# Kernel tuning notes

Measured on AMD Instinct MI355X. Metric: run time of the kernel, lower is better.

The kernel has to match this reference:

```python
import jax, jax.numpy as jnp
import numpy as np

DIM = 128
N_GNN = 3
B, N1, N2 = 8, 128, 512
VDW_N = 6.0
DEV_VDW = 0.2
MAX_VDW, MIN_VDW = 0.0356, 0.0178
DM_MIN = 0.5


def setup_inputs() -> dict:
    key = jax.random.key(0)
    ks = jax.random.split(key, 24)
    f32 = jnp.float32
    h1 = jax.random.normal(ks[0], (B, N1, 54), f32)
    h2 = jax.random.normal(ks[1], (B, N2, 54), f32)
    a1 = (jax.random.uniform(ks[2], (B, N1, N1)) < 0.1).astype(f32)
    adj1 = jnp.clip(a1 + jnp.swapaxes(a1, 1, 2) + jnp.eye(N1, dtype=f32), 0.0, 1.0)
    a2 = (jax.random.uniform(ks[3], (B, N2, N2)) < 0.05).astype(f32)
    adj2 = jnp.clip(a2 + jnp.swapaxes(a2, 1, 2) + jnp.eye(N2, dtype=f32), 0.0, 1.0)
    A_int = (jax.random.uniform(ks[4], (B, 8, N1, N2)) < 0.05).astype(f32)
    pos1 = jax.random.uniform(ks[5], (B, N1, 3), f32) * 30.0
    pos2 = jax.random.uniform(ks[6], (B, N2, 3), f32) * 30.0
    rotor = jax.random.uniform(ks[7], (B,), f32) * 10.0
    vdw_radius1 = 1.0 + jax.random.uniform(ks[8], (B, N1), f32)
    vdw_radius2 = 1.0 + jax.random.uniform(ks[9], (B, N2), f32)
    delta_uff = jax.random.uniform(ks[10], (B,), f32)
    no_metal1 = jnp.ones((B, N1), f32)
    no_metal2 = jnp.ones((B, N2), f32)
    s = 0.1
    node_W = jax.random.normal(ks[11], (54, DIM), f32) * s
    gat_W = jax.random.normal(ks[12], (N_GNN, DIM, DIM), f32) * s
    gat_b = jnp.zeros((N_GNN, DIM), f32)
    gat_A = jax.random.normal(ks[13], (N_GNN, DIM, DIM), f32) * s
    gate_W = jax.random.normal(ks[14], (N_GNN, 2 * DIM), f32) * s
    gate_b = jnp.zeros((N_GNN,), f32)
    vdwA_W1 = jax.random.normal(ks[15], (2 * DIM, 128), f32) * s
    vdwA_b1 = jnp.zeros((128,), f32)
    vdwA_W2 = jax.random.normal(ks[16], (128,), f32) * s
    vdwA_b2 = jnp.zeros((1,), f32)
    vdwB_W1 = jax.random.normal(ks[17], (2 * DIM, 128), f32) * s
    vdwB_b1 = jnp.zeros((128,), f32)
    vdwB_W2 = jax.random.normal(ks[18], (128,), f32) * s
    vdwB_b2 = jnp.zeros((1,), f32)
    hbond_coeff = jnp.array([1.0], f32)
    hydrophobic_coeff = jnp.array([0.5], f32)
    vdw_coeff = jnp.array([1.0], f32)
    rotor_coeff = jnp.array([0.5], f32)
    return dict(h1=h1, adj1=adj1, h2=h2, adj2=adj2, A_int=A_int, pos1=pos1, pos2=pos2,
                rotor=rotor, vdw_radius1=vdw_radius1, vdw_radius2=vdw_radius2,
                delta_uff=delta_uff, no_metal1=no_metal1, no_metal2=no_metal2,
                node_W=node_W, gat_W=gat_W, gat_b=gat_b, gat_A=gat_A, gate_W=gate_W,
                gate_b=gate_b, vdwA_W1=vdwA_W1, vdwA_b1=vdwA_b1, vdwA_W2=vdwA_W2,
                vdwA_b2=vdwA_b2, vdwB_W1=vdwB_W1, vdwB_b1=vdwB_b1, vdwB_W2=vdwB_W2,
                vdwB_b2=vdwB_b2, hbond_coeff=hbond_coeff,
                hydrophobic_coeff=hydrophobic_coeff, vdw_coeff=vdw_coeff,
                rotor_coeff=rotor_coeff)


def _gat(x, adj, W, b, A, gW, gb):
    # PIGNet GAT_gate: attention softmax over axis=1, masked by adj, gated residual.
    h = x @ W + b                                   # [B,N,D]
    e = jnp.einsum('bil,bkl->bik', h @ A, h)        # [B,N,N]
    e = e + jnp.swapaxes(e, 1, 2)
    att = jnp.where(adj > 0, e, -9e15)
    att = jax.nn.softmax(att, axis=1) * adj
    h_prime = jax.nn.relu(jnp.einsum('bij,bjk->bik', att, h))
    coeff = jax.nn.sigmoid(jnp.concatenate([x, h_prime], -1) @ gW + gb)[..., None]
    return coeff * x + (1.0 - coeff) * h_prime


def _pair_mlp(g1, g2, W1, b1, w2, b2):
    # Equivalent to Linear(cat[h1_rep,h2_rep]) without materializing the 2D concat.
    z = (jnp.einsum('bik,kh->bih', g1, W1[:DIM])[:, :, None, :]
         + jnp.einsum('bjk,kh->bjh', g2, W1[DIM:])[:, None, :, :] + b1)  # [B,N1,N2,128]
    return jax.nn.relu(z) @ w2 + b2                 # [B,N1,N2]


def _forward(h1, adj1, h2, adj2, A_int, pos1, pos2, rotor, vdw_radius1, vdw_radius2,
             delta_uff, no_metal1, no_metal2, node_W, gat_W, gat_b, gat_A, gate_W,
             gate_b, vdwA_W1, vdwA_b1, vdwA_W2, vdwA_b2, vdwB_W1, vdwB_b1, vdwB_W2,
             vdwB_b2, hbond_coeff, hydrophobic_coeff, vdw_coeff, rotor_coeff):
    g1 = h1 @ node_W
    g2 = h2 @ node_W
    for i in range(N_GNN):
        g1 = _gat(g1, adj1, gat_W[i], gat_b[i], gat_A[i], gate_W[i], gate_b[i])
        g2 = _gat(g2, adj2, gat_W[i], gat_b[i], gat_A[i], gate_W[i], gate_b[i])
    diff = pos1[:, :, None, :] - pos2[:, None, :, :]
    dm = jnp.sqrt(jnp.sum(diff * diff, -1) + 1e-10)   # [B,N1,N2]
    dm = jnp.where(dm < DM_MIN, 1e10, dm)
    A_w = jax.nn.sigmoid(_pair_mlp(g1, g2, vdwA_W1, vdwA_b1, vdwA_W2, vdwA_b2))
    B_w = jnp.tanh(_pair_mlp(g1, g2, vdwB_W1, vdwB_b1, vdwB_W2, vdwB_b2)) * DEV_VDW
    dm0 = vdw_radius1[:, :, None] + vdw_radius2[:, None, :] + B_w
    # vdW 12-6 term
    dm0_safe = jnp.where(dm0 < 1e-4, 1.0, dm0)
    rN = (dm0_safe / dm) ** VDW_N
    evdw = jnp.minimum(rN * rN - 2.0 * rN, 100.0)
    mask12 = no_metal1[:, :, None] * no_metal2[:, None, :]
    Aamp = A_w * (MAX_VDW - MIN_VDW) + MIN_VDW
    E_vdw = jnp.sum(Aamp * evdw * mask12, axis=(1, 2))
    # hbond / hydrophobic terms use unfixed dm0
    dmd = dm - dm0
    hb = -(hbond_coeff * hbond_coeff)[0]
    hy = -(hydrophobic_coeff * hydrophobic_coeff)[0]
    E_hb1 = jnp.sum(jnp.clip(dmd * A_int[:, 1] / -0.7, 0.0, 1.0), axis=(1, 2)) * hb
    E_hb2 = jnp.sum(jnp.clip(dmd * A_int[:, -1] / -0.7, 0.0, 1.0), axis=(1, 2)) * hb
    E_hp = jnp.sum(jnp.clip((-dmd + 1.5) * A_int[:, -2], 0.0, 1.0), axis=(1, 2)) * hy
    E_t = delta_uff * (vdw_coeff * vdw_coeff)[0]
    ret = jnp.stack([E_vdw, E_hb1, E_hb2, E_hp, E_t], -1)   # [B,5]
    ret = ret / (1.0 + (rotor_coeff * rotor_coeff)[0] * rotor[:, None])
    return ret


def reference(h1, adj1, h2, adj2, A_int, pos1, pos2, rotor, vdw_radius1, vdw_radius2,
              delta_uff, no_metal1, no_metal2, node_W, gat_W, gat_b, gat_A, gate_W,
              gate_b, vdwA_W1, vdwA_b1, vdwA_W2, vdwA_b2, vdwB_W1, vdwB_b1, vdwB_W2,
              vdwB_b2, hbond_coeff, hydrophobic_coeff, vdw_coeff, rotor_coeff):
    return _forward(h1, adj1, h2, adj2, A_int, pos1, pos2, rotor, vdw_radius1,
                    vdw_radius2, delta_uff, no_metal1, no_metal2, node_W, gat_W,
                    gat_b, gat_A, gate_W, gate_b, vdwA_W1, vdwA_b1, vdwA_W2,
                    vdwA_b2, vdwB_W1, vdwB_b1, vdwB_W2, vdwB_b2, hbond_coeff,
                    hydrophobic_coeff, vdw_coeff, rotor_coeff)
```

## Files before the change

kernel.cpp:

```cpp
#include <hip/hip_runtime.h>
#include <hip/hip_fp16.h>
#include <math.h>

#define D 128
#define NB 8
#define NN1 128
#define NN2 512
#define ROWS1 (NB * NN1)
#define ROWS2 (NB * NN2)
#define ROWS (ROWS1 + ROWS2)
#define CAP1 96
#define CAP2 160
#define CSR_ELEMS ((size_t)ROWS1 * CAP1 + (size_t)ROWS2 * CAP2)

typedef __half HT;

__device__ __forceinline__ void resolve_row(int row, int& base_row, size_t& cbase,
                                            int& N) {
    if (row < ROWS1) {
        base_row = row & ~127;
        cbase = (size_t)row * CAP1;
        N = NN1;
    } else {
        int r = row - ROWS1;
        base_row = ROWS1 + (r & ~511);
        cbase = (size_t)ROWS1 * CAP1 + (size_t)r * CAP2;
        N = NN2;
    }
}

__device__ __forceinline__ int swiz_row4(int bid) {
    int batch = bid & 7, gi = bid >> 3;
    return (gi < 32) ? batch * NN1 + gi * 4
                     : ROWS1 + batch * NN2 + (gi - 32) * 4;
}
__device__ __forceinline__ int swiz_row(int bid) {
    int batch = bid & 7, idx = bid >> 3;
    return (idx < NN1) ? batch * NN1 + idx
                       : ROWS1 + batch * NN2 + (idx - NN1);
}

__device__ __forceinline__ void load8h(const HT* p, float* o) {
    float4 raw = *(const float4*)p;
    const __half2* h2 = (const __half2*)&raw;
    float2 f0 = __half22float2(h2[0]);
    float2 f1 = __half22float2(h2[1]);
    float2 f2 = __half22float2(h2[2]);
    float2 f3 = __half22float2(h2[3]);
    o[0] = f0.x; o[1] = f0.y; o[2] = f1.x; o[3] = f1.y;
    o[4] = f2.x; o[5] = f2.y; o[6] = f3.x; o[7] = f3.y;
}

#define GEMM4(XS, W, BV, STMT0, STMT1)                                        \
    {                                                                         \
        float acc0 = (BV), acc1 = (BV);                                       \
        for (int k0 = 0; k0 < D; k0 += 4) {                                   \
            float w0 = (W)[(k0 + 0) * D + d];                                 \
            float w1 = (W)[(k0 + 1) * D + d];                                 \
            float w2 = (W)[(k0 + 2) * D + d];                                 \
            float w3 = (W)[(k0 + 3) * D + d];                                 \
            float4 x0 = *(const float4*)&XS[rh * 2 + 0][k0];                  \
            float4 x1 = *(const float4*)&XS[rh * 2 + 1][k0];                  \
            acc0 += x0.x * w0 + x0.y * w1 + x0.z * w2 + x0.w * w3;            \
            acc1 += x1.x * w0 + x1.y * w1 + x1.z * w2 + x1.w * w3;            \
        }                                                                     \
        STMT0; STMT1;                                                         \
    }

__global__ __launch_bounds__(256) void k_init(
    const float* __restrict__ h1in, const float* __restrict__ h2in,
    const float* __restrict__ adj1, const float* __restrict__ adj2,
    const float* __restrict__ nodeW, const float* __restrict__ W,
    const float* __restrict__ bias, const float* __restrict__ A,
    float* __restrict__ g, HT* __restrict__ hOut, HT* __restrict__ hAOut,
    unsigned short* __restrict__ csr, int* __restrict__ nnz,
    float* __restrict__ out) {
    int row0 = swiz_row4(blockIdx.x);
    int t = threadIdx.x;
    if (blockIdx.x == 0 && t < NB * 5) out[t] = 0.f;
    __shared__ float hin[4][54];
    __shared__ float xs[4][D];
    __shared__ float hs[4][D];
    {
        const float* src = (row0 < ROWS1) ? h1in + (size_t)row0 * 54
                                          : h2in + (size_t)(row0 - ROWS1) * 54;
        for (int idx = t; idx < 4 * 54; idx += 256) {
            int r = idx / 54, c = idx - r * 54;
            hin[r][c] = src[(size_t)r * 54 + c];
        }
    }
    __syncthreads();
    int d = t & 127, rh = t >> 7;
    {
        float e0 = 0.f, e1 = 0.f;
        for (int k = 0; k < 54; ++k) {
            float w = nodeW[k * D + d];
            e0 += hin[rh * 2 + 0][k] * w;
            e1 += hin[rh * 2 + 1][k] * w;
        }
        xs[rh * 2 + 0][d] = e0;
        xs[rh * 2 + 1][d] = e1;
        g[((size_t)row0 + rh * 2 + 0) * D + d] = e0;
        g[((size_t)row0 + rh * 2 + 1) * D + d] = e1;
    }
    __syncthreads();
    float bv = bias[d];
    GEMM4(xs, W, bv,
          { hs[rh * 2 + 0][d] = acc0;
            hOut[((size_t)row0 + rh * 2 + 0) * D + d] = __float2half(acc0); },
          { hs[rh * 2 + 1][d] = acc1;
            hOut[((size_t)row0 + rh * 2 + 1) * D + d] = __float2half(acc1); })
    __syncthreads();
    GEMM4(hs, A, 0.f,
          { hAOut[((size_t)row0 + rh * 2 + 0) * D + d] = __float2half(acc0); },
          { hAOut[((size_t)row0 + rh * 2 + 1) * D + d] = __float2half(acc1); })
    {
        int lane = t & 63, wv = t >> 6;
        int row = row0 + wv;
        int base_row, N;
        size_t cbase;
        resolve_row(row, base_row, cbase, N);
        int cap = (row < ROWS1) ? CAP1 : CAP2;
        const float* arow = (row < ROWS1) ? adj1 + (size_t)row * NN1
                                          : adj2 + (size_t)(row - ROWS1) * NN2;
        int cnt = 0;
        for (int c0 = 0; c0 < N; c0 += 64) {
            float v = arow[c0 + lane];
            unsigned long long m = __ballot(v > 0.f);
            int rank = __popcll(m & ((1ull << lane) - 1ull));
            if (v > 0.f && cnt + rank < cap)
                csr[cbase + cnt + rank] = (unsigned short)(c0 + lane);
            cnt += __popcll(m);
        }
        if (lane == 0) nnz[row] = cnt < cap ? cnt : cap;
    }
}

__global__ __launch_bounds__(128) void k_Ssp(const HT* __restrict__ h,
                                             const HT* __restrict__ hA,
                                             const unsigned short* __restrict__ csr,
                                             const int* __restrict__ nnz,
                                             float* __restrict__ svals,
                                             float2* __restrict__ rowstat) {
    int row = swiz_row(blockIdx.x);
    int t = threadIdx.x;
    int base_row, N;
    size_t cbase;
    resolve_row(row, base_row, cbase, N);
    int n = nnz[row];
    int grp = t >> 4, u = t & 15;
    float hi[8], ai[8];
    load8h(h + (size_t)row * D + u * 8, hi);
    load8h(hA + (size_t)row * D + u * 8, ai);
    __shared__ float sv[CAP2];
    for (int s0 = 0; s0 < n; s0 += 16) {
        int sa = s0 + grp;
        int sb = sa + 8;
        float pa = 0.f, pb = 0.f;
        if (sa < n) {
            int jrow = base_row + csr[cbase + sa];
            float hj[8], aj[8];
            load8h(h + (size_t)jrow * D + u * 8, hj);
            load8h(hA + (size_t)jrow * D + u * 8, aj);
#pragma unroll
            for (int q = 0; q < 8; ++q) pa += hi[q] * aj[q] + ai[q] * hj[q];
        }
        if (sb < n) {
            int jrow = base_row + csr[cbase + sb];
            float hj[8], aj[8];
            load8h(h + (size_t)jrow * D + u * 8, hj);
            load8h(hA + (size_t)jrow * D + u * 8, aj);
#pragma unroll
            for (int q = 0; q < 8; ++q) pb += hi[q] * aj[q] + ai[q] * hj[q];
        }
#pragma unroll
        for (int o = 8; o > 0; o >>= 1) {
            pa += __shfl_xor(pa, o);
            pb += __shfl_xor(pb, o);
        }
        if (u == 0) {
            if (sa < n) sv[sa] = pa;
            if (sb < n) sv[sb] = pb;
        }
    }
    __syncthreads();
    if (t < 64) {
        float m = -3.4e38f;
        for (int s = t; s < n; s += 64) m = fmaxf(m, sv[s]);
#pragma unroll
        for (int o = 32; o > 0; o >>= 1) m = fmaxf(m, __shfl_xor(m, o));
        float sum = 0.f;
        for (int s = t; s < n; s += 64) sum += expf(sv[s] - m);
#pragma unroll
        for (int o = 32; o > 0; o >>= 1) sum += __shfl_xor(sum, o);
        if (t == 0) rowstat[row] = make_float2(m, 1.f / sum);
    }
    for (int s = t; s < n; s += 128) svals[cbase + s] = sv[s];
}

__device__ __forceinline__ void gate4(
    int row0, int t, const HT* __restrict__ hIn, float* __restrict__ g,
    const float* __restrict__ svals, const float2* __restrict__ rowstat,
    const unsigned short* __restrict__ csr, const int* __restrict__ nnz,
    const float* __restrict__ gW, float gb0, float (*xs)[D],
    float av[4][CAP2], unsigned short ax[4][CAP2]) {
    int lane = t & 63, wv = t >> 6;
    int row = row0 + wv;
    int base_row, N;
    size_t cbase;
    resolve_row(row, base_row, cbase, N);
    int n = nnz[row];
    for (int s = lane; s < n; s += 64) {
        int jl = csr[cbase + s];
        float2 st = rowstat[base_row + jl];
        av[wv][s] = expf(svals[cbase + s] - st.x) * st.y;
        ax[wv][s] = (unsigned short)jl;
    }
    const __half2* hb2 = (const __half2*)hIn;
    size_t boff = ((size_t)base_row << 6) + lane;
    float2 a[8];
#pragma unroll
    for (int u = 0; u < 8; ++u) a[u] = make_float2(0.f, 0.f);
    int s = 0;
    for (; s + 8 <= n; s += 8) {
#pragma unroll
        for (int u = 0; u < 8; ++u) {
            float avv = av[wv][s + u];
            float2 f = __half22float2(hb2[boff + ((size_t)ax[wv][s + u] << 6)]);
            a[u].x += avv * f.x;
            a[u].y += avv * f.y;
        }
    }
    for (; s < n; ++s) {
        float avv = av[wv][s];
        float2 f = __half22float2(hb2[boff + ((size_t)ax[wv][s] << 6)]);
        a[0].x += avv * f.x;
        a[0].y += avv * f.y;
    }
    float hv0 = fmaxf(((a[0].x + a[1].x) + (a[2].x + a[3].x)) +
                      ((a[4].x + a[5].x) + (a[6].x + a[7].x)), 0.f);
    float hv1 = fmaxf(((a[0].y + a[1].y) + (a[2].y + a[3].y)) +
                      ((a[4].y + a[5].y) + (a[6].y + a[7].y)), 0.f);
    float2 xv = *(const float2*)&g[(size_t)row * D + 2 * lane];
    float2 w01 = *(const float2*)&gW[2 * lane];
    float2 w23 = *(const float2*)&gW[D + 2 * lane];
    float part = xv.x * w01.x + xv.y * w01.y + hv0 * w23.x + hv1 * w23.y;
#pragma unroll
    for (int o = 32; o > 0; o >>= 1) part += __shfl_xor(part, o);
    float c = 1.f / (1.f + expf(-(part + gb0)));
    float g0 = c * xv.x + (1.f - c) * hv0;
    float g1 = c * xv.y + (1.f - c) * hv1;
    xs[wv][2 * lane] = g0;
    xs[wv][2 * lane + 1] = g1;
    *(float2*)&g[(size_t)row * D + 2 * lane] = make_float2(g0, g1);
}

__global__ __launch_bounds__(256) void k_gh(
    const HT* __restrict__ hIn, float* __restrict__ g,
    const float* __restrict__ svals, const float2* __restrict__ rowstat,
    const unsigned short* __restrict__ csr, const int* __restrict__ nnz,
    const float* __restrict__ gW, const float* __restrict__ gb,
    const float* __restrict__ W, const float* __restrict__ bias,
    const float* __restrict__ A, HT* __restrict__ hOut, HT* __restrict__ hAOut) {
    int row0 = swiz_row4(blockIdx.x);
    int t = threadIdx.x;
    __shared__ float xs[4][D];
    __shared__ float hs[4][D];
    __shared__ float av[4][CAP2];
    __shared__ unsigned short ax[4][CAP2];
    gate4(row0, t, hIn, g, svals, rowstat, csr, nnz, gW, gb[0], xs, av, ax);
    __syncthreads();
    int d = t & 127, rh = t >> 7;
    float bv = bias[d];
    GEMM4(xs, W, bv,
          { hs[rh * 2 + 0][d] = acc0;
            hOut[((size_t)row0 + rh * 2 + 0) * D + d] = __float2half(acc0); },
          { hs[rh * 2 + 1][d] = acc1;
            hOut[((size_t)row0 + rh * 2 + 1) * D + d] = __float2half(acc1); })
    __syncthreads();
    GEMM4(hs, A, 0.f,
          { hAOut[((size_t)row0 + rh * 2 + 0) * D + d] = __float2half(acc0); },
          { hAOut[((size_t)row0 + rh * 2 + 1) * D + d] = __float2half(acc1); })
}

__global__ __launch_bounds__(256) void k_gp(
    const HT* __restrict__ hIn, float* __restrict__ g,
    const float* __restrict__ svals, const float2* __restrict__ rowstat,
    const unsigned short* __restrict__ csr, const int* __restrict__ nnz,
    const float* __restrict__ gW, const float* __restrict__ gb,
    const float* __restrict__ WA, const float* __restrict__ WB,
    const float* __restrict__ bA, const float* __restrict__ bB,
    float* __restrict__ aA, float* __restrict__ aB) {
    int row0 = swiz_row4(blockIdx.x);
    int t = threadIdx.x;
    __shared__ float xs[4][D];
    __shared__ float av[4][CAP2];
    __shared__ unsigned short ax[4][CAP2];
    gate4(row0, t, hIn, g, svals, rowstat, csr, nnz, gW, gb[0], xs, av, ax);
    __syncthreads();
    int d = t & 127, rh = t >> 7;
    int g2 = (row0 >= ROWS1);
    const float* WAp = g2 ? WA + D * D : WA;
    const float* WBp = g2 ? WB + D * D : WB;
    float bvA = g2 ? 0.f : bA[d];
    float bvB = g2 ? 0.f : bB[d];
    GEMM4(xs, WAp, bvA,
          { aA[((size_t)row0 + rh * 2 + 0) * D + d] = acc0; },
          { aA[((size_t)row0 + rh * 2 + 1) * D + d] = acc1; })
    GEMM4(xs, WBp, bvB,
          { aB[((size_t)row0 + rh * 2 + 0) * D + d] = acc0; },
          { aB[((size_t)row0 + rh * 2 + 1) * D + d] = acc1; })
}

__global__ __launch_bounds__(256) void k_pairz(
    const float* __restrict__ aA, const float* __restrict__ aB,
    const float* __restrict__ w2A, const float* __restrict__ w2B,
    const float* __restrict__ b2A, const float* __restrict__ b2B,
    const float* __restrict__ pos1, const float* __restrict__ pos2,
    const float* __restrict__ vr1, const float* __restrict__ vr2,
    const float* __restrict__ nm1, const float* __restrict__ nm2,
    const float* __restrict__ A_int, const float* __restrict__ rotor,
    const float* __restrict__ duff, const float* __restrict__ hbond,
    const float* __restrict__ hydro, const float* __restrict__ vdwc,
    const float* __restrict__ rotc, float* __restrict__ out) {
    int b = blockIdx.x & 7;
    int tile = blockIdx.x >> 3;
    int itile = tile >> 4, jtile = tile & 15;
    int i0 = itile * 32, j0 = jtile * 32;
    int t = threadIdx.x;
    int tx = t & 15, ty = t >> 4;
    __shared__ float A1a[32][20], A1b[32][20], A2a[32][20], A2b[32][20];
    __shared__ float w2As[128], w2Bs[128];
    __shared__ float zAs[32][33], zBs[32][33];
    __shared__ float redc[8][4];
    if (t < 128) { w2As[t] = w2A[t]; w2Bs[t] = w2B[t]; }
    float zA[2][2] = {{0.f, 0.f}, {0.f, 0.f}};
    float zB[2][2] = {{0.f, 0.f}, {0.f, 0.f}};
    int half = t >> 7, idx = t & 127;
    int sr = idx >> 2, sc = (idx & 3) * 4;
    size_t grow = half ? (size_t)(ROWS1 + b * NN2 + j0 + sr)
                       : (size_t)(b * NN1 + i0 + sr);
    for (int hc = 0; hc < D; hc += 16) {
        __syncthreads();
        float4 va = *(const float4*)&aA[grow * D + hc + sc];
        float4 vb = *(const float4*)&aB[grow * D + hc + sc];
        if (half) { *(float4*)&A2a[sr][sc] = va; *(float4*)&A2b[sr][sc] = vb; }
        else      { *(float4*)&A1a[sr][sc] = va; *(float4*)&A1b[sr][sc] = vb; }
        __syncthreads();
#pragma unroll
        for (int hh = 0; hh < 16; hh += 4) {
            float4 wA = *(const float4*)&w2As[hc + hh];
            float4 wB = *(const float4*)&w2Bs[hc + hh];
            float4 xA0 = *(const float4*)&A1a[ty][hh];
            float4 xA1 = *(const float4*)&A1a[ty + 16][hh];
            float4 xB0 = *(const float4*)&A1b[ty][hh];
            float4 xB1 = *(const float4*)&A1b[ty + 16][hh];
            float4 yA0 = *(const float4*)&A2a[tx][hh];
            float4 yA1 = *(const float4*)&A2a[tx + 16][hh];
            float4 yB0 = *(const float4*)&A2b[tx][hh];
            float4 yB1 = *(const float4*)&A2b[tx + 16][hh];
#define RD4(xx, yy, ww) (fmaxf(xx.x + yy.x, 0.f) * ww.x + fmaxf(xx.y + yy.y, 0.f) * ww.y + \
                         fmaxf(xx.z + yy.z, 0.f) * ww.z + fmaxf(xx.w + yy.w, 0.f) * ww.w)
            zA[0][0] += RD4(xA0, yA0, wA); zA[0][1] += RD4(xA0, yA1, wA);
            zA[1][0] += RD4(xA1, yA0, wA); zA[1][1] += RD4(xA1, yA1, wA);
            zB[0][0] += RD4(xB0, yB0, wB); zB[0][1] += RD4(xB0, yB1, wB);
            zB[1][0] += RD4(xB1, yB0, wB); zB[1][1] += RD4(xB1, yB1, wB);
#undef RD4
        }
    }
#pragma unroll
    for (int u = 0; u < 2; ++u)
#pragma unroll
        for (int v = 0; v < 2; ++v) {
            zAs[ty + 16 * u][tx + 16 * v] = zA[u][v];
            zBs[ty + 16 * u][tx + 16 * v] = zB[u][v];
        }
    __syncthreads();
    int j2 = t & 31, ig = t >> 5;
    int jg = j0 + j2;
    size_t j_off = (size_t)b * NN2 + jg;
    float p2x = pos2[j_off * 3 + 0], p2y = pos2[j_off * 3 + 1], p2z = pos2[j_off * 3 + 2];
    float r2 = vr2[j_off], m2 = nm2[j_off];
    float zb2A = b2A[0], zb2B = b2B[0];
    float eV[4], e1[4], e2[4], eH[4];
#pragma unroll
    for (int ii = 0; ii < 4; ++ii) {
        int il = ig * 4 + ii;
        int iglob = i0 + il;
        size_t i_off = (size_t)b * NN1 + iglob;
        float zAv = zAs[il][j2] + zb2A;
        float zBv = zBs[il][j2] + zb2B;
        float dx = pos1[i_off * 3 + 0] - p2x;
        float dy = pos1[i_off * 3 + 1] - p2y;
        float dz = pos1[i_off * 3 + 2] - p2z;
        float dm = sqrtf(dx * dx + dy * dy + dz * dz + 1e-10f);
        if (dm < 0.5f) dm = 1e10f;
        float A_w = 1.f / (1.f + expf(-zAv));
        float B_w = tanhf(zBv) * 0.2f;
        float dm0 = vr1[i_off] + r2 + B_w;
        float dm0s = (dm0 < 1e-4f) ? 1.f : dm0;
        float rr = dm0s / dm;
        float rr2 = rr * rr;
        float rN = rr2 * rr2 * rr2;
        float evdw = fminf(rN * rN - 2.f * rN, 100.f);
        float mask = nm1[i_off] * m2;
        float Aamp = A_w * (0.0356f - 0.0178f) + 0.0178f;
        eV[ii] = Aamp * evdw * mask;
        float dmd = dm - dm0;
        size_t abase = (((size_t)b * 8) * NN1 + iglob) * NN2 + jg;
        float Ai1 = A_int[abase + (size_t)1 * NN1 * NN2];
        float Ai6 = A_int[abase + (size_t)6 * NN1 * NN2];
        float Ai7 = A_int[abase + (size_t)7 * NN1 * NN2];
        e1[ii] = fminf(fmaxf(dmd * Ai1 * (-1.f / 0.7f), 0.f), 1.f);
        e2[ii] = fminf(fmaxf(dmd * Ai7 * (-1.f / 0.7f), 0.f), 1.f);
        eH[ii] = fminf(fmaxf((1.5f - dmd) * Ai6, 0.f), 1.f);
    }
    float sV = (eV[0] + eV[1]) + (eV[2] + eV[3]);
    float s1 = (e1[0] + e1[1]) + (e1[2] + e1[3]);
    float s2 = (e2[0] + e2[1]) + (e2[2] + e2[3]);
    float sH = (eH[0] + eH[1]) + (eH[2] + eH[3]);
#pragma unroll
    for (int o = 16; o > 0; o >>= 1) {
        sV += __shfl_xor(sV, o);
        s1 += __shfl_xor(s1, o);
        s2 += __shfl_xor(s2, o);
        sH += __shfl_xor(sH, o);
    }
    if (j2 == 0) {
        redc[ig][0] = sV; redc[ig][1] = s1; redc[ig][2] = s2; redc[ig][3] = sH;
    }
    __syncthreads();
    if (t < 4) {
        float v = 0.f;
#pragma unroll
        for (int gg = 0; gg < 8; ++gg) v += redc[gg][t];
        float scl = 1.f / (1.f + rotc[0] * rotc[0] * rotor[b]);
        float coef;
        if (t == 0) coef = scl;
        else if (t == 3) coef = -hydro[0] * hydro[0] * scl;
        else coef = -hbond[0] * hbond[0] * scl;
        atomicAdd(&out[b * 5 + t], v * coef);
    }
    if (t == 4 && tile == 0) {
        float scl = 1.f / (1.f + rotc[0] * rotc[0] * rotor[b]);
        atomicAdd(&out[b * 5 + 4], duff[b] * vdwc[0] * vdwc[0] * scl);
    }
}

extern "C" void kernel_launch(void* const* d_in, const int* in_sizes, int n_in,
                              void* d_out, int out_size, void* d_ws, size_t ws_size,
                              hipStream_t stream) {
    const float* h1    = (const float*)d_in[0];
    const float* adj1  = (const float*)d_in[1];
    const float* h2    = (const float*)d_in[2];
    const float* adj2  = (const float*)d_in[3];
    const float* A_int = (const float*)d_in[4];
    const float* pos1  = (const float*)d_in[5];
    const float* pos2  = (const float*)d_in[6];
    const float* rotor = (const float*)d_in[7];
    const float* vr1   = (const float*)d_in[8];
    const float* vr2   = (const float*)d_in[9];
    const float* duff  = (const float*)d_in[10];
    const float* nm1   = (const float*)d_in[11];
    const float* nm2   = (const float*)d_in[12];
    const float* nodeW = (const float*)d_in[13];
    const float* gatW  = (const float*)d_in[14];
    const float* gatb  = (const float*)d_in[15];
    const float* gatA  = (const float*)d_in[16];
    const float* gateW = (const float*)d_in[17];
    const float* gateb = (const float*)d_in[18];
    const float* vA_W1 = (const float*)d_in[19];
    const float* vA_b1 = (const float*)d_in[20];
    const float* vA_W2 = (const float*)d_in[21];
    const float* vA_b2 = (const float*)d_in[22];
    const float* vB_W1 = (const float*)d_in[23];
    const float* vB_b1 = (const float*)d_in[24];
    const float* vB_W2 = (const float*)d_in[25];
    const float* vB_b2 = (const float*)d_in[26];
    const float* hbond = (const float*)d_in[27];
    const float* hydro = (const float*)d_in[28];
    const float* vdwc  = (const float*)d_in[29];
    const float* rotc  = (const float*)d_in[30];

    float* p = (float*)d_ws;
    float* g     = p; p += (size_t)ROWS * D;
    float* aA    = p; p += (size_t)ROWS * D;
    float* aB    = p; p += (size_t)ROWS * D;
    float* svals = p; p += CSR_ELEMS;
    float2* rowstat = (float2*)p; p += 2 * (size_t)ROWS;
    HT* hb0 = (HT*)p; p += (size_t)ROWS * D / 2;
    HT* hA0 = (HT*)p; p += (size_t)ROWS * D / 2;
    HT* hb1 = (HT*)p; p += (size_t)ROWS * D / 2;
    HT* hA1 = (HT*)p; p += (size_t)ROWS * D / 2;
    unsigned short* csr = (unsigned short*)p;
    int* nnz = (int*)(csr + CSR_ELEMS);
    float* outp = (float*)d_out;

    k_init<<<ROWS / 4, 256, 0, stream>>>(h1, h2, adj1, adj2, nodeW, gatW, gatb, gatA,
                                         g, hb0, hA0, csr, nnz, outp);
    k_Ssp<<<ROWS, 128, 0, stream>>>(hb0, hA0, csr, nnz, svals, rowstat);
    k_gh<<<ROWS / 4, 256, 0, stream>>>(hb0, g, svals, rowstat, csr, nnz,
                                       gateW, gateb,
                                       gatW + (size_t)1 * D * D, gatb + D,
                                       gatA + (size_t)1 * D * D, hb1, hA1);
    k_Ssp<<<ROWS, 128, 0, stream>>>(hb1, hA1, csr, nnz, svals, rowstat);
    k_gh<<<ROWS / 4, 256, 0, stream>>>(hb1, g, svals, rowstat, csr, nnz,
                                       gateW + 2 * D, gateb + 1,
                                       gatW + (size_t)2 * D * D, gatb + 2 * D,
                                       gatA + (size_t)2 * D * D, hb0, hA0);
    k_Ssp<<<ROWS, 128, 0, stream>>>(hb0, hA0, csr, nnz, svals, rowstat);
    k_gp<<<ROWS / 4, 256, 0, stream>>>(hb0, g, svals, rowstat, csr, nnz,
                                       gateW + 4 * D, gateb + 2,
                                       vA_W1, vB_W1, vA_b1, vB_b1, aA, aB);

    k_pairz<<<512, 256, 0, stream>>>(aA, aB, vA_W2, vB_W2, vA_b2, vB_b2,
                                     pos1, pos2, vr1, vr2, nm1, nm2, A_int,
                                     rotor, duff, hbond, hydro, vdwc, rotc, outp);
}
```

Baseline: 261.5 us.

## Pack two rows per Ssp block, skip final g store, prefetch pair loads

k_Ssp now processes two rows per 256-thread block instead of one row per 128-thread block, halving block count and sharing launch overhead. The last gating kernel no longer writes g back to global memory since it is not consumed afterward. In k_pairz, per-i position, radius, mask and A_int loads are hoisted before the shared-memory store and barrier so their latency overlaps the sync. Risks: rows of different nnz in the same block cause imbalance, and extra registers in k_pairz may reduce occupancy.

Measured after the change: 257.2 us. No clear change (-1.6%).

```diff
diff --git a/kernel.cpp b/kernel.cpp
--- a/kernel.cpp
+++ b/kernel.cpp
@@ -34,10 +34,10 @@
     return (gi < 32) ? batch * NN1 + gi * 4
                      : ROWS1 + batch * NN2 + (gi - 32) * 4;
 }
-__device__ __forceinline__ int swiz_row(int bid) {
-    int batch = bid & 7, idx = bid >> 3;
-    return (idx < NN1) ? batch * NN1 + idx
-                       : ROWS1 + batch * NN2 + (idx - NN1);
+__device__ __forceinline__ int swiz_row2(int bid) {
+    int batch = bid & 7, gi = bid >> 3;
+    return (gi < 64) ? batch * NN1 + gi * 2
+                     : ROWS1 + batch * NN2 + (gi - 64) * 2;
 }
 
 __device__ __forceinline__ void load8h(const HT* p, float* o) {
@@ -136,23 +136,24 @@
     }
 }
 
-__global__ __launch_bounds__(128) void k_Ssp(const HT* __restrict__ h,
+__global__ __launch_bounds__(256) void k_Ssp(const HT* __restrict__ h,
                                              const HT* __restrict__ hA,
                                              const unsigned short* __restrict__ csr,
                                              const int* __restrict__ nnz,
                                              float* __restrict__ svals,
                                              float2* __restrict__ rowstat) {
-    int row = swiz_row(blockIdx.x);
     int t = threadIdx.x;
+    int half = t >> 7, t2 = t & 127;
+    int row = swiz_row2(blockIdx.x) + half;
     int base_row, N;
     size_t cbase;
     resolve_row(row, base_row, cbase, N);
     int n = nnz[row];
-    int grp = t >> 4, u = t & 15;
+    int grp = t2 >> 4, u = t2 & 15;
     float hi[8], ai[8];
     load8h(h + (size_t)row * D + u * 8, hi);
     load8h(hA + (size_t)row * D + u * 8, ai);
-    __shared__ float sv[CAP2];
+    __shared__ float sv[2][CAP2];
     for (int s0 = 0; s0 < n; s0 += 16) {
         int sa = s0 + grp;
         int sb = sa + 8;
@@ -179,23 +180,23 @@
             pb += __shfl_xor(pb, o);
         }
         if (u == 0) {
-            if (sa < n) sv[sa] = pa;
-            if (sb < n) sv[sb] = pb;
-        }
-    }
-    __syncthreads();
-    if (t < 64) {
+            if (sa < n) sv[half][sa] = pa;
+            if (sb < n) sv[half][sb] = pb;
+        }
+    }
+    __syncthreads();
+    if (t2 < 64) {
         float m = -3.4e38f;
-        for (int s = t; s < n; s += 64) m = fmaxf(m, sv[s]);
+        for (int s = t2; s < n; s += 64) m = fmaxf(m, sv[half][s]);
 #pragma unroll
         for (int o = 32; o > 0; o >>= 1) m = fmaxf(m, __shfl_xor(m, o));
         float sum = 0.f;
-        for (int s = t; s < n; s += 64) sum += expf(sv[s] - m);
+        for (int s = t2; s < n; s += 64) sum += expf(sv[half][s] - m);
 #pragma unroll
         for (int o = 32; o > 0; o >>= 1) sum += __shfl_xor(sum, o);
-        if (t == 0) rowstat[row] = make_float2(m, 1.f / sum);
-    }
-    for (int s = t; s < n; s += 128) svals[cbase + s] = sv[s];
+        if (t2 == 0) rowstat[row] = make_float2(m, 1.f / sum);
+    }
+    for (int s = t2; s < n; s += 128) svals[cbase + s] = sv[half][s];
 }
 
 __device__ __forceinline__ void gate4(
@@ -203,7 +204,7 @@
     const float* __restrict__ svals, const float2* __restrict__ rowstat,
     const unsigned short* __restrict__ csr, const int* __restrict__ nnz,
     const float* __restrict__ gW, float gb0, float (*xs)[D],
-    float av[4][CAP2], unsigned short ax[4][CAP2]) {
+    float av[4][CAP2], unsigned short ax[4][CAP2], int writeG) {
     int lane = t & 63, wv = t >> 6;
     int row = row0 + wv;
     int base_row, N;
@@ -252,7 +253,7 @@
     float g1 = c * xv.y + (1.f - c) * hv1;
     xs[wv][2 * lane] = g0;
     xs[wv][2 * lane + 1] = g1;
-    *(float2*)&g[(size_t)row * D + 2 * lane] = make_float2(g0, g1);
+    if (writeG) *(float2*)&g[(size_t)row * D + 2 * lane] = make_float2(g0, g1);
 }
 
 __global__ __launch_bounds__(256) void k_gh(
@@ -268,7 +269,7 @@
     __shared__ float hs[4][D];
     __shared__ float av[4][CAP2];
     __shared__ unsigned short ax[4][CAP2];
-    gate4(row0, t, hIn, g, svals, rowstat, csr, nnz, gW, gb[0], xs, av, ax);
+    gate4(row0, t, hIn, g, svals, rowstat, csr, nnz, gW, gb[0], xs, av, ax, 1);
     __syncthreads();
     int d = t & 127, rh = t >> 7;
     float bv = bias[d];
@@ -296,7 +297,7 @@
     __shared__ float xs[4][D];
     __shared__ float av[4][CAP2];
     __shared__ unsigned short ax[4][CAP2];
-    gate4(row0, t, hIn, g, svals, rowstat, csr, nnz, gW, gb[0], xs, av, ax);
+    gate4(row0, t, hIn, g, svals, rowstat, csr, nnz, gW, gb[0], xs, av, ax, 0);
     __syncthreads();
     int d = t & 127, rh = t >> 7;
     int g2 = (row0 >= ROWS1);
@@ -368,52 +369,61 @@
 #undef RD4
         }
     }
-#pragma unroll
-    for (int u = 0; u < 2; ++u)
-#pragma unroll
-        for (int v = 0; v < 2; ++v) {
-            zAs[ty + 16 * u][tx + 16 * v] = zA[u][v];
-            zBs[ty + 16 * u][tx + 16 * v] = zB[u][v];
-        }
-    __syncthreads();
     int j2 = t & 31, ig = t >> 5;
     int jg = j0 + j2;
     size_t j_off = (size_t)b * NN2 + jg;
     float p2x = pos2[j_off * 3 + 0], p2y = pos2[j_off * 3 + 1], p2z = pos2[j_off * 3 + 2];
     float r2 = vr2[j_off], m2 = nm2[j_off];
     float zb2A = b2A[0], zb2B = b2B[0];
+    float Ai1r[4], Ai6r[4], Ai7r[4], p1xr[4], p1yr[4], p1zr[4], vr1r[4], nm1r[4];
+#pragma unroll
+    for (int ii = 0; ii < 4; ++ii) {
+        int iglob = i0 + ig * 4 + ii;
+        size_t i_off = (size_t)b * NN1 + iglob;
+        p1xr[ii] = pos1[i_off * 3 + 0];
+        p1yr[ii] = pos1[i_off * 3 + 1];
+        p1zr[ii] = pos1[i_off * 3 + 2];
+        vr1r[ii] = vr1[i_off];
+        nm1r[ii] = nm1[i_off];
+        size_t abase = (((size_t)b * 8) * NN1 + iglob) * NN2 + jg;
+        Ai1r[ii] = A_int[abase + (size_t)1 * NN1 * NN2];
+        Ai6r[ii] = A_int[abase + (size_t)6 * NN1 * NN2];
+        Ai7r[ii] = A_int[abase + (size_t)7 * NN1 * NN2];
+    }
+#pragma unroll
+    for (int u = 0; u < 2; ++u)
+#pragma unroll
+        for (int v = 0; v < 2; ++v) {
+            zAs[ty + 16 * u][tx + 16 * v] = zA[u][v];
+            zBs[ty + 16 * u][tx + 16 * v] = zB[u][v];
+        }
+    __syncthreads();
     float eV[4], e1[4], e2[4], eH[4];
 #pragma unroll
     for (int ii = 0; ii < 4; ++ii) {
         int il = ig * 4 + ii;
-        int iglob = i0 + il;
-        size_t i_off = (size_t)b * NN1 + iglob;
         float zAv = zAs[il][j2] + zb2A;
         float zBv = zBs[il][j2] + zb2B;
-        float dx = pos1[i_off * 3 + 0] - p2x;
-        float dy = pos1[i_off * 3 + 1] - p2y;
-        float dz = pos1[i_off * 3 + 2] - p2z;
+        float dx = p1xr[ii] - p2x;
+        float dy = p1yr[ii] - p2y;
+        float dz = p1zr[ii] - p2z;
         float dm = sqrtf(dx * dx + dy * dy + dz * dz + 1e-10f);
         if (dm < 0.5f) dm = 1e10f;
         float A_w = 1.f / (1.f + expf(-zAv));
         float B_w = tanhf(zBv) * 0.2f;
-        float dm0 = vr1[i_off] + r2 + B_w;
+        float dm0 = vr1r[ii] + r2 + B_w;
         float dm0s = (dm0 < 1e-4f) ? 1.f : dm0;
         float rr = dm0s / dm;
         float rr2 = rr * rr;
         float rN = rr2 * rr2 * rr2;
         float evdw = fminf(rN * rN - 2.f * rN, 100.f);
-        float mask = nm1[i_off] * m2;
+        float mask = nm1r[ii] * m2;
         float Aamp = A_w * (0.0356f - 0.0178f) + 0.0178f;
         eV[ii] = Aamp * evdw * mask;
         float dmd = dm - dm0;
-        size_t abase = (((size_t)b * 8) * NN1 + iglob) * NN2 + jg;
-        float Ai1 = A_int[abase + (size_t)1 * NN1 * NN2];
-        float Ai6 = A_int[abase + (size_t)6 * NN1 * NN2];
-        float Ai7 = A_int[abase + (size_t)7 * NN1 * NN2];
-        e1[ii] = fminf(fmaxf(dmd * Ai1 * (-1.f / 0.7f), 0.f), 1.f);
-        e2[ii] = fminf(fmaxf(dmd * Ai7 * (-1.f / 0.7f), 0.f), 1.f);
-        eH[ii] = fminf(fmaxf((1.5f - dmd) * Ai6, 0.f), 1.f);
+        e1[ii] = fminf(fmaxf(dmd * Ai1r[ii] * (-1.f / 0.7f), 0.f), 1.f);
+        e2[ii] = fminf(fmaxf(dmd * Ai7r[ii] * (-1.f / 0.7f), 0.f), 1.f);
+        eH[ii] = fminf(fmaxf((1.5f - dmd) * Ai6r[ii], 0.f), 1.f);
     }
     float sV = (eV[0] + eV[1]) + (eV[2] + eV[3]);
     float s1 = (e1[0] + e1[1]) + (e1[2] + e1[3]);
@@ -498,17 +508,17 @@
 
     k_init<<<ROWS / 4, 256, 0, stream>>>(h1, h2, adj1, adj2, nodeW, gatW, gatb, gatA,
                                          g, hb0, hA0, csr, nnz, outp);
-    k_Ssp<<<ROWS, 128, 0, stream>>>(hb0, hA0, csr, nnz, svals, rowstat);
+    k_Ssp<<<ROWS / 2, 256, 0, stream>>>(hb0, hA0, csr, nnz, svals, rowstat);
     k_gh<<<ROWS / 4, 256, 0, stream>>>(hb0, g, svals, rowstat, csr, nnz,
                                        gateW, gateb,
                                        gatW + (size_t)1 * D * D, gatb + D,
                                        gatA + (size_t)1 * D * D, hb1, hA1);
-    k_Ssp<<<ROWS, 128, 0, stream>>>(hb1, hA1, csr, nnz, svals, rowstat);
+    k_Ssp<<<ROWS / 2, 256, 0, stream>>>(hb1, hA1, csr, nnz, svals, rowstat);
     k_gh<<<ROWS / 4, 256, 0, stream>>>(hb1, g, svals, rowstat, csr, nnz,
                                        gateW + 2 * D, gateb + 1,
                                        gatW + (size_t)2 * D * D, gatb + 2 * D,
                                        gatA + (size_t)2 * D * D, hb0, hA0);
-    k_Ssp<<<ROWS, 128, 0, stream>>>(hb0, hA0, csr, nnz, svals, rowstat);
+    k_Ssp<<<ROWS / 2, 256, 0, stream>>>(hb0, hA0, csr, nnz, svals, rowstat);
     k_gp<<<ROWS / 4, 256, 0, stream>>>(hb0, g, svals, rowstat, csr, nnz,
                                        gateW + 4 * D, gateb + 2,
                                        vA_W1, vB_W1, vA_b1, vB_b1, aA, aB);
```
